# Kernel optimization log

Measured on AMD Instinct MI355X. Metric: run time of the kernel, lower is better.

The kernel has to match this reference:

```python
import jax, jax.numpy as jnp
import numpy as np

D = 1024        # hidden_size
H = 16          # num_heads
HD = D // H     # head_dim = 64
K = 4           # conv kernel size
I = int(D * 2.7)  # ffn intermediate = 2764
B, T = 2, 2048
EPS = 1e-6
GATE_BIAS = 4.0


def setup_inputs() -> dict:
    key = jax.random.key(0)
    ks = jax.random.split(key, 16)
    s = D ** -0.5
    return {
        "x": jax.random.normal(ks[0], (B, T, D), jnp.float32),
        "norm1_w": jnp.ones((D,), jnp.float32),
        "norm2_w": jnp.ones((D,), jnp.float32),
        "conv_w": jax.random.normal(ks[1], (D, K), jnp.float32) * 0.2,
        "conv_b": jnp.zeros((D,), jnp.float32),
        "wq": jax.random.normal(ks[2], (D, D), jnp.float32) * s,
        "wk": jax.random.normal(ks[3], (D, D), jnp.float32) * s,
        "wv": jax.random.normal(ks[4], (D, D), jnp.float32) * s,
        "wb": jax.random.normal(ks[5], (D, H), jnp.float32) * s,
        "wa": jax.random.normal(ks[6], (D, H), jnp.float32) * s,
        "wo": jax.random.normal(ks[7], (D, D), jnp.float32) * s,
        "wg": jax.random.normal(ks[8], (D, I), jnp.float32) * s,
        "wu": jax.random.normal(ks[9], (D, I), jnp.float32) * s,
        "wd": jax.random.normal(ks[10], (I, D), jnp.float32) * (I ** -0.5),
    }


def _rmsnorm(x, w):
    return x * jax.lax.rsqrt(jnp.mean(x * x, axis=-1, keepdims=True) + EPS) * w


def _causal_depthwise_conv(x, conv_w, conv_b):
    # x: [B,T,D]; depthwise causal conv, kernel K, then SiLU
    xt = jnp.transpose(x, (0, 2, 1))  # [B,D,T]
    y = jax.lax.conv_general_dilated(
        xt, conv_w[:, None, :],  # [D,1,K]
        window_strides=(1,), padding=[(K - 1, 0)],
        feature_group_count=D,
        dimension_numbers=("NCH", "OIH", "NCH"))
    y = jnp.transpose(y, (0, 2, 1)) + conv_b  # [B,T,D]
    return jax.nn.silu(y)


def _l2norm(x):
    return x * jax.lax.rsqrt(jnp.sum(x * x, axis=-1, keepdims=True) + EPS)


def _gated_delta_rule(xc, wq, wk, wv, wb, wa):
    b, t = xc.shape[0], xc.shape[1]
    q = _l2norm((xc @ wq).reshape(b, t, H, HD))
    k = _l2norm((xc @ wk).reshape(b, t, H, HD))
    v = (xc @ wv).reshape(b, t, H, HD)
    beta = jax.nn.sigmoid(xc @ wb)              # [B,T,H]
    alpha = jax.nn.sigmoid(xc @ wa + GATE_BIAS)  # [B,T,H] decay gate

    # time-major for scan
    qt = jnp.moveaxis(q, 1, 0)
    kt = jnp.moveaxis(k, 1, 0)
    vt = jnp.moveaxis(v, 1, 0)
    bt = jnp.moveaxis(beta, 1, 0)
    at = jnp.moveaxis(alpha, 1, 0)

    S0 = jnp.zeros((b, H, HD, HD), xc.dtype)  # [B,H,dk,dv]

    def step(S, inp):
        q_, k_, v_, b_, a_ = inp
        S = a_[..., None, None] * S
        pred = jnp.einsum("bhkv,bhk->bhv", S, k_)
        S = S + k_[..., :, None] * (b_[..., None] * (v_ - pred))[..., None, :]
        o = jnp.einsum("bhkv,bhk->bhv", S, q_)
        return S, o

    _, o = jax.lax.scan(step, S0, (qt, kt, vt, bt, at))  # [T,B,H,HD]
    return jnp.moveaxis(o, 1, 0).reshape(b, t, D)


def reference(x, norm1_w, norm2_w, conv_w, conv_b, wq, wk, wv, wb, wa, wo,
              wg, wu, wd):
    residual = x
    xn = _rmsnorm(x, norm1_w)
    xc = _causal_depthwise_conv(xn, conv_w, conv_b)
    mixer_out = _gated_delta_rule(xc, wq, wk, wv, wb, wa) @ wo
    h = residual + mixer_out
    hn = _rmsnorm(h, norm2_w)
    ffn = (jax.nn.silu(hn @ wg) * (hn @ wu)) @ wd
    return h + ffn
```

## Files before the change

### kernel.cpp

```cpp
#include <hip/hip_runtime.h>
#include <math.h>

#define D_ 1024
#define H_ 16
#define HD_ 64
#define KW_ 4
#define I_ 2764
#define IP_ 2816
#define NQKV_ 3200
#define NGU_ 5632
#define B_ 2
#define T_ 2048
#define BT_ (B_*T_)
#define ND_ (BT_*D_)
#define NH_ (BT_*H_)
#define NCH_ 32
#define NG_ (32*NCH_)
#define EPS_ 1e-6f
#define GATE_BIAS_ 4.0f

typedef __attribute__((ext_vector_type(8))) short bf16x8;
typedef __attribute__((ext_vector_type(4))) float f32x4;

#define MFMA_(a,b,c) __builtin_amdgcn_mfma_f32_16x16x32_bf16(a, b, c, 0, 0, 0)
#define GLDS_(src, dst) __builtin_amdgcn_global_load_lds( \
    (const __attribute__((address_space(1))) void*)(src), \
    (__attribute__((address_space(3))) void*)(dst), 16, 0, 0)

__device__ float f_sc1[BT_];
__device__ float f_be[NH_];
__device__ float f_al[NH_];
__device__ float f_h[ND_];
__device__ float g_rs[NG_ * 256];
__device__ float g_BmT[(size_t)NG_*4096];
__device__ unsigned short g_Gqk[(size_t)NG_*4096];
__device__ unsigned short g_Y[(size_t)NG_*4096];
__device__ unsigned short g_ZT[(size_t)NG_*4096];
__device__ unsigned short g_A[(size_t)NG_*4096];
__device__ unsigned short g_S[(size_t)NG_*4096];
__device__ unsigned short b_q[ND_];
__device__ unsigned short b_k[ND_];
__device__ unsigned short b_v[ND_];
__device__ unsigned short b_xc[ND_];
__device__ unsigned short b_o[ND_];
__device__ unsigned short b_hn[ND_];
__device__ unsigned short b_f[(size_t)BT_*IP_];
__device__ unsigned short b_wqkvT[(size_t)NQKV_*D_];
__device__ unsigned short b_woT[D_*D_];
__device__ unsigned short b_wguT[(size_t)NGU_*D_];
__device__ unsigned short b_wdT[(size_t)D_*IP_];

__device__ __forceinline__ unsigned short f2b(float x) {
  union { float f; unsigned u; } a; a.f = x;
  unsigned r = a.u + 0x7fff + ((a.u >> 16) & 1);
  return (unsigned short)(r >> 16);
}
__device__ __forceinline__ float b2f(unsigned short s) {
  union { unsigned u; float f; } a; a.u = ((unsigned)s) << 16; return a.f;
}

__device__ __forceinline__ const unsigned short* bsel(int id) {
  switch (id) {
    case 0: return b_xc;  case 1: return b_o;    case 2: return b_hn;
    case 3: return b_f;   case 4: return b_wqkvT; case 5: return b_woT;
    case 6: return b_wguT; default: return b_wdT;
  }
}
__device__ __forceinline__ unsigned short* bselw(int id) {
  return (unsigned short*)bsel(id);
}

__global__ __launch_bounds__(256) void rmssc_k(const float* __restrict__ x) {
  int row = blockIdx.x;
  int tid = threadIdx.x;
  float4 v = ((const float4*)(x + (size_t)row * D_))[tid];
  float ss = v.x*v.x + v.y*v.y + v.z*v.z + v.w*v.w;
  #pragma unroll
  for (int o = 32; o > 0; o >>= 1) ss += __shfl_down(ss, o);
  __shared__ float sred[4];
  if ((tid & 63) == 0) sred[tid >> 6] = ss;
  __syncthreads();
  if (tid == 0)
    f_sc1[row] = rsqrtf((sred[0]+sred[1]+sred[2]+sred[3]) / (float)D_ + EPS_);
}

__global__ __launch_bounds__(256) void rms2_k(const float* __restrict__ w) {
  int row = blockIdx.x;
  const float* xr = f_h + (size_t)row * D_;
  int tid = threadIdx.x;
  float4 v = ((const float4*)xr)[tid];
  float ss = v.x*v.x + v.y*v.y + v.z*v.z + v.w*v.w;
  #pragma unroll
  for (int o = 32; o > 0; o >>= 1) ss += __shfl_down(ss, o);
  __shared__ float sred[4];
  __shared__ float sscale;
  if ((tid & 63) == 0) sred[tid >> 6] = ss;
  __syncthreads();
  if (tid == 0)
    sscale = rsqrtf((sred[0]+sred[1]+sred[2]+sred[3]) / (float)D_ + EPS_);
  __syncthreads();
  float s = sscale;
  float4 wv = ((const float4*)w)[tid];
  unsigned short* orow = b_hn + (size_t)row * D_ + tid * 4;
  orow[0] = f2b(v.x*s*wv.x); orow[1] = f2b(v.y*s*wv.y);
  orow[2] = f2b(v.z*s*wv.z); orow[3] = f2b(v.w*s*wv.w);
}

__global__ __launch_bounds__(256) void conv2_k(const float* __restrict__ x,
                                               const float* __restrict__ cw,
                                               const float* __restrict__ cb,
                                               const float* __restrict__ n1w) {
  int idx = blockIdx.x * 256 + threadIdx.x;
  int d = idx & (D_ - 1);
  int bt = idx >> 10;
  int t = bt & (T_ - 1);
  float wd = n1w[d];
  float acc = cb[d];
  #pragma unroll
  for (int j = 0; j < KW_; j++) {
    int tt = t - (KW_ - 1) + j;
    if (tt >= 0) {
      int off = j - (KW_ - 1);
      acc += x[(size_t)idx + (size_t)off * D_] * f_sc1[bt + off] * wd * cw[d * KW_ + j];
    }
  }
  float s = acc / (1.f + expf(-acc));
  b_xc[idx] = f2b(s);
}

__global__ __launch_bounds__(256) void castTqkv_k(const float* __restrict__ wq,
                                                  const float* __restrict__ wk,
                                                  const float* __restrict__ wv,
                                                  const float* __restrict__ wb,
                                                  const float* __restrict__ wa) {
  __shared__ float s[64][65];
  int n0 = blockIdx.x * 64, k0 = blockIdx.y * 64;
  int tx = threadIdx.x & 63, ty = threadIdx.x >> 6;
  int nn = n0 + tx;
  const float* src = nullptr; int col = 0, ld = 1024;
  if (nn < 1024)      { src = wq; col = nn; }
  else if (nn < 2048) { src = wk; col = nn - 1024; }
  else if (nn < 3072) { src = wv; col = nn - 2048; }
  else if (nn < 3088) { src = wb; col = nn - 3072; ld = 16; }
  else if (nn < 3104) { src = wa; col = nn - 3088; ld = 16; }
  #pragma unroll
  for (int j = ty; j < 64; j += 4)
    s[j][tx] = src ? src[(size_t)(k0 + j) * ld + col] : 0.f;
  __syncthreads();
  #pragma unroll
  for (int j = ty; j < 64; j += 4)
    b_wqkvT[(size_t)(n0 + j) * D_ + k0 + tx] = f2b(s[tx][j]);
}

__global__ __launch_bounds__(256) void castTgu_k(const float* __restrict__ wg,
                                                 const float* __restrict__ wu) {
  __shared__ float s[64][65];
  int n0 = blockIdx.x * 64, k0 = blockIdx.y * 64;
  int tx = threadIdx.x & 63, ty = threadIdx.x >> 6;
  int nn = n0 + tx;
  int inner = nn & 31;
  int col = (nn >> 5) * 16 + (inner & 15);
  const float* src = (inner < 16) ? wg : wu;
  bool ok = (col < I_);
  #pragma unroll
  for (int j = ty; j < 64; j += 4)
    s[j][tx] = ok ? src[(size_t)(k0 + j) * I_ + col] : 0.f;
  __syncthreads();
  #pragma unroll
  for (int j = ty; j < 64; j += 4)
    b_wguT[(size_t)(n0 + j) * D_ + k0 + tx] = f2b(s[tx][j]);
}

__global__ __launch_bounds__(256) void castT_k(const float* __restrict__ W,
                                               int K, int N, int outid, int Kp) {
  __shared__ float s[64][65];
  unsigned short* out = bselw(outid);
  int k0 = blockIdx.y * 64, n0 = blockIdx.x * 64;
  int tx = threadIdx.x & 63, ty = threadIdx.x >> 6;
  #pragma unroll
  for (int j = ty; j < 64; j += 4) {
    int kk = k0 + j, nn = n0 + tx;
    s[j][tx] = (kk < K && nn < N) ? W[(size_t)kk * N + nn] : 0.f;
  }
  __syncthreads();
  #pragma unroll
  for (int j = ty; j < 64; j += 4)
    out[(size_t)(n0 + j) * Kp + k0 + tx] = f2b(s[tx][j]);
}

__global__ __launch_bounds__(256) void gemm_bf16(int aid, int bid, int Kp, int mode,
                                                 const float* __restrict__ ext,
                                                 float* __restrict__ eout) {
  __shared__ __align__(16) unsigned short Al[3][128 * 32];
  __shared__ __align__(16) unsigned short Bl[3][128 * 32];
  const unsigned short* A = bsel(aid);
  const unsigned short* Bt = bsel(bid);
  int tid = threadIdx.x;
  int nbx = gridDim.x;
  int nwg = nbx * gridDim.y;
  int lid = blockIdx.y * nbx + blockIdx.x;
  int cpx = nwg >> 3;
  int swzb = (lid & 7) * cpx + (lid >> 3);
  int m0 = (swzb / nbx) * 128, n0 = (swzb % nbx) * 128;
  int wave = tid >> 6, lane = tid & 63;
  int wm = (wave >> 1) * 64, wn = (wave & 1) * 64;
  int lrow = tid >> 2;
  int lcol = ((tid & 3) ^ ((lrow >> 1) & 3)) * 8;
  f32x4 acc[4][4] = {};
  const int l15 = lane & 15, lg = lane >> 4;
  const int sw = (lg ^ ((l15 >> 1) & 3)) * 8;
  const int nt = Kp >> 5;
  const unsigned short* Arow = A + (size_t)m0 * Kp;
  const unsigned short* Brow = Bt + (size_t)n0 * Kp;
  {
    GLDS_(Arow + (size_t)lrow * Kp + lcol,        Al[0] + wave * 512);
    GLDS_(Arow + (size_t)(64 + lrow) * Kp + lcol, Al[0] + 2048 + wave * 512);
    GLDS_(Brow + (size_t)lrow * Kp + lcol,        Bl[0] + wave * 512);
    GLDS_(Brow + (size_t)(64 + lrow) * Kp + lcol, Bl[0] + 2048 + wave * 512);
    GLDS_(Arow + (size_t)lrow * Kp + 32 + lcol,        Al[1] + wave * 512);
    GLDS_(Arow + (size_t)(64 + lrow) * Kp + 32 + lcol, Al[1] + 2048 + wave * 512);
    GLDS_(Brow + (size_t)lrow * Kp + 32 + lcol,        Bl[1] + wave * 512);
    GLDS_(Brow + (size_t)(64 + lrow) * Kp + 32 + lcol, Bl[1] + 2048 + wave * 512);
  }
  int c0i = 0, c1i = 1, c2i = 2;
  for (int t = 0; t < nt; t++) {
    if (t + 2 < nt) {
      int k0 = (t + 2) << 5;
      GLDS_(Arow + (size_t)lrow * Kp + k0 + lcol,        Al[c2i] + wave * 512);
      GLDS_(Arow + (size_t)(64 + lrow) * Kp + k0 + lcol, Al[c2i] + 2048 + wave * 512);
      GLDS_(Brow + (size_t)lrow * Kp + k0 + lcol,        Bl[c2i] + wave * 512);
      GLDS_(Brow + (size_t)(64 + lrow) * Kp + k0 + lcol, Bl[c2i] + 2048 + wave * 512);
      asm volatile("s_waitcnt vmcnt(8)" ::: "memory");
    } else if (t + 1 < nt) {
      asm volatile("s_waitcnt vmcnt(4)" ::: "memory");
    } else {
      asm volatile("s_waitcnt vmcnt(0)" ::: "memory");
    }
    __builtin_amdgcn_sched_barrier(0);
    __builtin_amdgcn_s_barrier();
    __builtin_amdgcn_sched_barrier(0);
    bf16x8 af[4], bf[4];
    #pragma unroll
    for (int i = 0; i < 4; i++)
      af[i] = *(const bf16x8*)&Al[c0i][(wm + i * 16 + l15) * 32 + sw];
    #pragma unroll
    for (int j = 0; j < 4; j++)
      bf[j] = *(const bf16x8*)&Bl[c0i][(wn + j * 16 + l15) * 32 + sw];
    #pragma unroll
    for (int i = 0; i < 4; i++)
      #pragma unroll
      for (int j = 0; j < 4; j++)
        acc[i][j] = MFMA_(af[i], bf[j], acc[i][j]);
    __builtin_amdgcn_sched_barrier(0);
    __builtin_amdgcn_s_barrier();
    __builtin_amdgcn_sched_barrier(0);
    int tmp = c0i; c0i = c1i; c1i = c2i; c2i = tmp;
  }
  int C0 = n0 + wn;
  if (mode == 0) {
    if (C0 < 2048) {
      unsigned short* dst = (C0 < 1024) ? b_q : b_k;
      int cbase = C0 & 1023;
      #pragma unroll
      for (int i = 0; i < 4; i++) {
        int r0i = m0 + wm + i * 16 + lg * 4;
        #pragma unroll
        for (int r = 0; r < 4; r++) {
          float ss = acc[i][0][r]*acc[i][0][r] + acc[i][1][r]*acc[i][1][r]
                   + acc[i][2][r]*acc[i][2][r] + acc[i][3][r]*acc[i][3][r];
          ss += __shfl_xor(ss, 1); ss += __shfl_xor(ss, 2);
          ss += __shfl_xor(ss, 4); ss += __shfl_xor(ss, 8);
          float sc = rsqrtf(ss + EPS_);
          #pragma unroll
          for (int j = 0; j < 4; j++)
            dst[(size_t)(r0i + r) * D_ + cbase + j * 16 + l15] = f2b(acc[i][j][r] * sc);
        }
      }
    } else if (C0 < 3072) {
      int cbase = C0 & 1023;
      #pragma unroll
      for (int i = 0; i < 4; i++) {
        int r0i = m0 + wm + i * 16 + lg * 4;
        #pragma unroll
        for (int j = 0; j < 4; j++)
          #pragma unroll
          for (int r = 0; r < 4; r++)
            b_v[(size_t)(r0i + r) * D_ + cbase + j * 16 + l15] = f2b(acc[i][j][r]);
      }
    } else if (C0 == 3072) {
      #pragma unroll
      for (int i = 0; i < 4; i++) {
        int r0i = m0 + wm + i * 16 + lg * 4;
        #pragma unroll
        for (int r = 0; r < 4; r++) {
          float vb = acc[i][0][r];
          f_be[(size_t)(r0i + r) * H_ + l15] = 1.f / (1.f + expf(-vb));
          float va = acc[i][1][r] + GATE_BIAS_;
          f_al[(size_t)(r0i + r) * H_ + l15] = 1.f / (1.f + expf(-va));
        }
      }
    }
  } else if (mode == 1) {
    #pragma unroll
    for (int i = 0; i < 4; i++) {
      int r0i = m0 + wm + i * 16 + lg * 4;
      #pragma unroll
      for (int jp = 0; jp < 2; jp++) {
        int j = jp * 2;
        int Lbase = ((C0 + j * 16) >> 5) * 16;
        #pragma unroll
        for (int r = 0; r < 4; r++) {
          float g = acc[i][j][r], u = acc[i][j + 1][r];
          float sg = g / (1.f + expf(-g));
          b_f[(size_t)(r0i + r) * IP_ + Lbase + l15] = f2b(sg * u);
        }
      }
    }
  } else if (mode == 2) {
    #pragma unroll
    for (int i = 0; i < 4; i++) {
      int r0i = m0 + wm + i * 16 + lg * 4;
      #pragma unroll
      for (int j = 0; j < 4; j++)
        #pragma unroll
        for (int r = 0; r < 4; r++) {
          size_t off = (size_t)(r0i + r) * D_ + C0 + j * 16 + l15;
          f_h[off] = ext[off] + acc[i][j][r];
        }
    }
  } else {
    #pragma unroll
    for (int i = 0; i < 4; i++) {
      int r0i = m0 + wm + i * 16 + lg * 4;
      #pragma unroll
      for (int j = 0; j < 4; j++)
        #pragma unroll
        for (int r = 0; r < 4; r++) {
          size_t off = (size_t)(r0i + r) * D_ + C0 + j * 16 + l15;
          eout[off] = f_h[off] + acc[i][j][r];
        }
    }
  }
}


__global__ __launch_bounds__(256) void prep_k() {
  __shared__ __align__(16) char sm[40448];
  unsigned short* sKT = (unsigned short*)sm;
  unsigned short* sVT = (unsigned short*)(sm + 10240);
  unsigned short* sAb = (unsigned short*)(sm + 20480);
  unsigned short* sYT = (unsigned short*)(sm + 20480);
  unsigned short* sXb = (unsigned short*)(sm + 29696);
  float* sL  = (float*)(sm + 38912);
  float* sB  = (float*)(sm + 39168);
  float* sS2 = (float*)(sm + 39424);
  float* sDec= (float*)(sm + 39680);
  float* sGC = (float*)(sm + 39936);

  int gid = blockIdx.x;
  int ch = gid & 31, bh = gid >> 5;
  int b = bh >> 4, h = bh & 15;
  int c0 = ch * 64, hb = h * HD_;
  int rowb = b * T_ + c0;
  int tid = threadIdx.x;
  int w = tid >> 6, lane = tid & 63, l15 = lane & 15, lg = lane >> 4;
  size_t g4 = (size_t)gid * 4096;

  if (tid < 64) {
    size_t rb = ((size_t)(rowb + tid)) * H_ + h;
    float la = log2f(f_al[rb]);
    #pragma unroll
    for (int m = 1; m < 64; m <<= 1) {
      float o = __shfl_up(la, m);
      if (tid >= m) la += o;
    }
    float L63 = __shfl(la, 63);
    float bt = f_be[rb];
    float g = exp2f(la);
    sL[tid] = la; sB[tid] = bt; sS2[tid] = bt * g;
    sDec[tid] = exp2f(L63 - la);
    if (tid == 63) sGC[0] = g;
    g_rs[(size_t)gid*256 + tid*4 + 0] = bt;
    g_rs[(size_t)gid*256 + tid*4 + 1] = bt * g;
    g_rs[(size_t)gid*256 + tid*4 + 2] = g;
  }
  __syncthreads();

  {
    int tp = tid >> 3, q8 = tid & 7;
    int t0 = 2 * tp, t1 = 2 * tp + 1;
    const bf16x8 k0 = *(const bf16x8*)(b_k + (size_t)(rowb + t0) * D_ + hb + q8 * 8);
    const bf16x8 k1 = *(const bf16x8*)(b_k + (size_t)(rowb + t1) * D_ + hb + q8 * 8);
    const bf16x8 v0 = *(const bf16x8*)(b_v + (size_t)(rowb + t0) * D_ + hb + q8 * 8);
    const bf16x8 v1 = *(const bf16x8*)(b_v + (size_t)(rowb + t1) * D_ + hb + q8 * 8);
    float s0 = sB[t0], s1v = sB[t1];
    unsigned* KT32 = (unsigned*)sKT;
    unsigned* VT32 = (unsigned*)sVT;
    #pragma unroll
    for (int i = 0; i < 8; i++) {
      int k = q8 * 8 + i;
      KT32[k*40 + tp] = (unsigned)(unsigned short)k0[i] |
                        ((unsigned)(unsigned short)k1[i] << 16);
      unsigned lo = f2b(b2f((unsigned short)v0[i]) * s0);
      unsigned hi = f2b(b2f((unsigned short)v1[i]) * s1v);
      VT32[k*40 + tp] = lo | (hi << 16);
    }
  }
  {
    bf16x8 bK[2], aK[4][2], aQ[4][2];
    #pragma unroll
    for (int k2 = 0; k2 < 2; k2++) {
      bK[k2] = *(const bf16x8*)&b_k[(size_t)(rowb + w*16 + l15)*D_ + hb + k2*32 + lg*8];
      #pragma unroll
      for (int ti = 0; ti < 4; ti++) {
        aK[ti][k2] = *(const bf16x8*)&b_k[(size_t)(rowb + ti*16 + l15)*D_ + hb + k2*32 + lg*8];
        aQ[ti][k2] = *(const bf16x8*)&b_q[(size_t)(rowb + ti*16 + l15)*D_ + hb + k2*32 + lg*8];
      }
    }
    f32x4 ck[4] = {}, cq[4] = {};
    #pragma unroll
    for (int k2 = 0; k2 < 2; k2++)
      #pragma unroll
      for (int ti = 0; ti < 4; ti++) {
        ck[ti] = MFMA_(aK[ti][k2], bK[k2], ck[ti]);
        cq[ti] = MFMA_(aQ[ti][k2], bK[k2], cq[ti]);
      }
    int j = w*16 + l15;
    float Lj = sL[j];
    #pragma unroll
    for (int ti = 0; ti < 4; ti++)
      #pragma unroll
      for (int r = 0; r < 4; r++) {
        int t = ti*16 + lg*4 + r;
        float ratio = exp2f(sL[t] - Lj);
        sAb[t*72 + j] = f2b((j < t) ? sB[t] * ratio * ck[ti][r] : 0.f);
        g_Gqk[g4 + t*64 + j] = f2b((j <= t) ? ratio * cq[ti][r] : 0.f);
      }
  }
  __syncthreads();
  {
    int c = (w << 4) + (lane >> 2);
    int p = lane & 3;
    int rb16 = p << 4;
    float xr[16];
    #pragma unroll
    for (int j = 0; j < 16; j++) xr[j] = 0.f;
    #pragma unroll
    for (int q = 0; q < 16; q++) {
      int r0 = 4 * q;
      const unsigned short* abr = sAb + r0 * 72 + rb16;
      bf16x8 A0a = *(const bf16x8*)(abr);
      bf16x8 A0b = *(const bf16x8*)(abr + 8);
      bf16x8 A1a = *(const bf16x8*)(abr + 72);
      bf16x8 A1b = *(const bf16x8*)(abr + 80);
      bf16x8 A2a = *(const bf16x8*)(abr + 144);
      bf16x8 A2b = *(const bf16x8*)(abr + 152);
      bf16x8 A3a = *(const bf16x8*)(abr + 216);
      bf16x8 A3b = *(const bf16x8*)(abr + 224);
      float s0 = 0.f, s1 = 0.f, s2 = 0.f, s3 = 0.f;
      #pragma unroll
      for (int j = 0; j < 8; j++) {
        float xv = xr[j], xw = xr[8 + j];
        s0 = fmaf(b2f((unsigned short)A0a[j]), xv, s0);
        s1 = fmaf(b2f((unsigned short)A1a[j]), xv, s1);
        s2 = fmaf(b2f((unsigned short)A2a[j]), xv, s2);
        s3 = fmaf(b2f((unsigned short)A3a[j]), xv, s3);
        s0 = fmaf(b2f((unsigned short)A0b[j]), xw, s0);
        s1 = fmaf(b2f((unsigned short)A1b[j]), xw, s1);
        s2 = fmaf(b2f((unsigned short)A2b[j]), xw, s2);
        s3 = fmaf(b2f((unsigned short)A3b[j]), xw, s3);
      }
      s0 += __shfl_xor(s0, 1); s0 += __shfl_xor(s0, 2);
      s1 += __shfl_xor(s1, 1); s1 += __shfl_xor(s1, 2);
      s2 += __shfl_xor(s2, 1); s2 += __shfl_xor(s2, 2);
      s3 += __shfl_xor(s3, 1); s3 += __shfl_xor(s3, 2);
      float a10 = b2f(sAb[(r0+1)*72 + r0]);
      float a20 = b2f(sAb[(r0+2)*72 + r0]);
      float a21 = b2f(sAb[(r0+2)*72 + r0+1]);
      float a30 = b2f(sAb[(r0+3)*72 + r0]);
      float a31 = b2f(sAb[(r0+3)*72 + r0+1]);
      float a32 = b2f(sAb[(r0+3)*72 + r0+2]);
      float x0 = ((r0+0) == c ? 1.f : 0.f) - s0;
      float x1 = ((r0+1) == c ? 1.f : 0.f) - s1 - a10*x0;
      float x2 = ((r0+2) == c ? 1.f : 0.f) - s2 - a20*x0 - a21*x1;
      float x3 = ((r0+3) == c ? 1.f : 0.f) - s3 - a30*x0 - a31*x1 - a32*x2;
      if (p == (q >> 2)) {
        int ji = 4 * (q & 3);
        xr[ji+0] = x0; xr[ji+1] = x1; xr[ji+2] = x2; xr[ji+3] = x3;
      }
    }
    #pragma unroll
    for (int j = 0; j < 16; j++)
      sXb[(rb16 + j)*72 + c] = f2b(xr[j]);
  }
  __syncthreads();
  int m0 = w * 16;
  f32x4 cyT[4], cz[4];
  {
    bf16x8 aKT[2];
    aKT[0] = *(const bf16x8*)&sKT[(m0 + l15)*80 + lg*8];
    aKT[1] = *(const bf16x8*)&sKT[(m0 + l15)*80 + 32 + lg*8];
    #pragma unroll
    for (int n = 0; n < 4; n++) {
      cyT[n] = f32x4{0.f, 0.f, 0.f, 0.f};
      #pragma unroll
      for (int k2 = 0; k2 < 2; k2++) {
        bf16x8 bb;
        #pragma unroll
        for (int i = 0; i < 8; i++) {
          int tp = k2*32 + lg*8 + i;
          bb[i] = (short)f2b(b2f(sXb[(n*16 + l15)*72 + tp]) * sS2[tp]);
        }
        cyT[n] = MFMA_(aKT[k2], bb, cyT[n]);
      }
    }
    bf16x8 aT2[2];
    #pragma unroll
    for (int k2 = 0; k2 < 2; k2++)
      #pragma unroll
      for (int i = 0; i < 8; i++) {
        int tp = k2*32 + lg*8 + i;
        aT2[k2][i] = (short)f2b(b2f(sXb[(m0 + l15)*72 + tp]) * sS2[tp]);
      }
    #pragma unroll
    for (int n = 0; n < 4; n++) {
      f32x4 c = {};
      #pragma unroll
      for (int k2 = 0; k2 < 2; k2++) {
        bf16x8 bKT = *(const bf16x8*)&sKT[(n*16 + l15)*80 + k2*32 + lg*8];
        c = MFMA_(aT2[k2], bKT, c);
      }
      #pragma unroll
      for (int r = 0; r < 4; r++)
        g_Y[g4 + (m0 + lg*4 + r)*64 + n*16 + l15] = f2b(c[r]);
    }
    bf16x8 aV[2];
    aV[0] = *(const bf16x8*)&sVT[(m0 + l15)*80 + lg*8];
    aV[1] = *(const bf16x8*)&sVT[(m0 + l15)*80 + 32 + lg*8];
    #pragma unroll
    for (int n = 0; n < 4; n++) {
      cz[n] = f32x4{0.f, 0.f, 0.f, 0.f};
      #pragma unroll
      for (int k2 = 0; k2 < 2; k2++) {
        bf16x8 bT = *(const bf16x8*)&sXb[(n*16 + l15)*72 + k2*32 + lg*8];
        cz[n] = MFMA_(aV[k2], bT, cz[n]);
      }
      #pragma unroll
      for (int r = 0; r < 4; r++)
        g_ZT[g4 + (m0 + lg*4 + r)*64 + n*16 + l15] = f2b(cz[n][r]);
    }
  }
  __syncthreads();
  #pragma unroll
  for (int n = 0; n < 4; n++)
    #pragma unroll
    for (int r = 0; r < 4; r++) {
      sYT[(m0 + lg*4 + r)*72 + n*16 + l15] = f2b(cyT[n][r]);
      sVT[(m0 + lg*4 + r)*80 + n*16 + l15] = f2b(cz[n][r]);
    }
  {
    int xx = tid >> 2, q = tid & 3;
    bf16x8 v0 = *(const bf16x8*)&sKT[xx*80 + q*16];
    bf16x8 v1 = *(const bf16x8*)&sKT[xx*80 + q*16 + 8];
    bf16x8 d0, d1;
    #pragma unroll
    for (int i = 0; i < 8; i++) {
      d0[i] = (short)f2b(b2f((unsigned short)v0[i]) * sDec[q*16 + i]);
      d1[i] = (short)f2b(b2f((unsigned short)v1[i]) * sDec[q*16 + 8 + i]);
    }
    *(bf16x8*)&sKT[xx*80 + q*16] = d0;
    *(bf16x8*)&sKT[xx*80 + q*16 + 8] = d1;
  }
  __syncthreads();
  {
    float gC = sGC[0];
    bf16x8 aKd[2];
    aKd[0] = *(const bf16x8*)&sKT[(m0 + l15)*80 + lg*8];
    aKd[1] = *(const bf16x8*)&sKT[(m0 + l15)*80 + 32 + lg*8];
    #pragma unroll
    for (int n = 0; n < 4; n++) {
      f32x4 c = {};
      #pragma unroll
      for (int k2 = 0; k2 < 2; k2++) {
        bf16x8 bY = *(const bf16x8*)&sYT[(n*16 + l15)*72 + k2*32 + lg*8];
        c = MFMA_(aKd[k2], bY, c);
      }
      #pragma unroll
      for (int r = 0; r < 4; r++) {
        int row = m0 + lg*4 + r, col = n*16 + l15;
        g_A[g4 + row*64 + col] = f2b(((row == col) ? gC : 0.f) - c[r]);
      }
    }
    #pragma unroll
    for (int n = 0; n < 4; n++) {
      f32x4 c = {};
      #pragma unroll
      for (int k2 = 0; k2 < 2; k2++) {
        bf16x8 bZ = *(const bf16x8*)&sVT[(n*16 + l15)*80 + k2*32 + lg*8];
        c = MFMA_(aKd[k2], bZ, c);
      }
      *(f32x4*)&g_BmT[g4 + (size_t)(n*16 + l15)*64 + m0 + lg*4] = c;
    }
  }
}

__global__ __launch_bounds__(256) void seq_k() {
  __shared__ __align__(16) unsigned short sST[4][16*80];
  int bh = blockIdx.x;
  int tid = threadIdx.x, w = tid >> 6, lane = tid & 63;
  int l15 = lane & 15, lg = lane >> 4;
  unsigned short* st = sST[w];
  for (int i = lane; i < 16*80; i += 64) st[i] = 0;
  f32x4 cerr[4] = {};
  bf16x8 aA[4][2];
  f32x4 cini[4];
  size_t g40 = (size_t)(bh * 32) * 4096;
  #pragma unroll
  for (int m = 0; m < 4; m++) {
    aA[m][0] = *(const bf16x8*)&g_A[g40 + (m*16 + l15)*64 + lg*8];
    aA[m][1] = *(const bf16x8*)&g_A[g40 + (m*16 + l15)*64 + 32 + lg*8];
    cini[m] = *(const f32x4*)&g_BmT[g40 + (w*16 + l15)*64 + m*16 + lg*4];
  }
  for (int ch = 0; ch < NCH_; ch++) {
    size_t gid = (size_t)bh * 32 + ch;
    float gC = g_rs[gid*256 + 254];
    bf16x8 bS0 = *(const bf16x8*)&st[l15*80 + lg*8];
    bf16x8 bS1 = *(const bf16x8*)&st[l15*80 + 32 + lg*8];
    *(bf16x8*)&g_S[gid*4096 + (w*16 + l15)*64 + lg*8] = bS0;
    *(bf16x8*)&g_S[gid*4096 + (w*16 + l15)*64 + 32 + lg*8] = bS1;
    bf16x8 aAn[4][2];
    f32x4 cin2[4];
    if (ch + 1 < NCH_) {
      size_t g4n = (gid + 1) * 4096;
      #pragma unroll
      for (int m = 0; m < 4; m++) {
        aAn[m][0] = *(const bf16x8*)&g_A[g4n + (m*16 + l15)*64 + lg*8];
        aAn[m][1] = *(const bf16x8*)&g_A[g4n + (m*16 + l15)*64 + 32 + lg*8];
        cin2[m] = *(const f32x4*)&g_BmT[g4n + (w*16 + l15)*64 + m*16 + lg*4];
      }
    }
    f32x4 c[4];
    #pragma unroll
    for (int m = 0; m < 4; m++) {
      #pragma unroll
      for (int r = 0; r < 4; r++)
        c[m][r] = cini[m][r] + gC * cerr[m][r];
      c[m] = MFMA_(aA[m][0], bS0, c[m]);
      c[m] = MFMA_(aA[m][1], bS1, c[m]);
    }
    #pragma unroll
    for (int m = 0; m < 4; m++)
      #pragma unroll
      for (int r = 0; r < 4; r++) {
        float x = c[m][r];
        unsigned short q = f2b(x);
        cerr[m][r] = x - b2f(q);
        st[l15*80 + m*16 + lg*4 + r] = q;
      }
    if (ch + 1 < NCH_) {
      #pragma unroll
      for (int m = 0; m < 4; m++) {
        aA[m][0] = aAn[m][0]; aA[m][1] = aAn[m][1];
        cini[m] = cin2[m];
      }
    }
  }
}

__global__ __launch_bounds__(256) void apply_k() {
  __shared__ __align__(16) unsigned short sUT[4][16*80];
  int gid = blockIdx.x;
  int ch = gid & 31, bh = gid >> 5;
  int b = bh >> 4, h = bh & 15;
  int c0 = ch * 64, hb = h * HD_;
  int rowb = b * T_ + c0;
  int tid = threadIdx.x, w = tid >> 6, lane = tid & 63;
  int l15 = lane & 15, lg = lane >> 4;
  unsigned short* ut = sUT[w];
  size_t g4 = (size_t)gid * 4096;
  bf16x8 aS[2];
  aS[0] = *(const bf16x8*)&g_S[g4 + (w*16 + l15)*64 + lg*8];
  aS[1] = *(const bf16x8*)&g_S[g4 + (w*16 + l15)*64 + 32 + lg*8];
  f32x4 cu[4];
  #pragma unroll
  for (int n = 0; n < 4; n++) {
    cu[n] = f32x4{0.f, 0.f, 0.f, 0.f};
    #pragma unroll
    for (int k2 = 0; k2 < 2; k2++) {
      bf16x8 bY = *(const bf16x8*)&g_Y[g4 + (n*16 + l15)*64 + k2*32 + lg*8];
      cu[n] = MFMA_(aS[k2], bY, cu[n]);
    }
  }
  #pragma unroll
  for (int n = 0; n < 4; n++)
    #pragma unroll
    for (int r = 0; r < 4; r++) {
      float zt = b2f(g_ZT[g4 + (w*16 + lg*4 + r)*64 + n*16 + l15]);
      ut[(lg*4 + r)*80 + n*16 + l15] = f2b(zt - cu[n][r]);
    }
  bf16x8 aU[2];
  aU[0] = *(const bf16x8*)&ut[l15*80 + lg*8];
  aU[1] = *(const bf16x8*)&ut[l15*80 + 32 + lg*8];
  f32x4 co[4];
  #pragma unroll
  for (int n = 0; n < 4; n++) {
    co[n] = f32x4{0.f, 0.f, 0.f, 0.f};
    #pragma unroll
    for (int k2 = 0; k2 < 2; k2++) {
      bf16x8 bQ = *(const bf16x8*)&b_q[(size_t)(rowb + n*16 + l15)*D_ + hb + k2*32 + lg*8];
      co[n] = MFMA_(aS[k2], bQ, co[n]);
    }
    float gm = g_rs[(size_t)gid*256 + (n*16 + l15)*4 + 2];
    #pragma unroll
    for (int r = 0; r < 4; r++) co[n][r] *= gm;
    #pragma unroll
    for (int k2 = 0; k2 < 2; k2++) {
      bf16x8 bG = *(const bf16x8*)&g_Gqk[g4 + (n*16 + l15)*64 + k2*32 + lg*8];
      co[n] = MFMA_(aU[k2], bG, co[n]);
    }
    ushort4 pk;
    pk.x = f2b(co[n][0]); pk.y = f2b(co[n][1]);
    pk.z = f2b(co[n][2]); pk.w = f2b(co[n][3]);
    *(ushort4*)&b_o[(size_t)(rowb + n*16 + l15)*D_ + hb + w*16 + lg*4] = pk;
  }
}

extern "C" void kernel_launch(void* const* d_in, const int* in_sizes, int n_in,
                              void* d_out, int out_size, void* d_ws, size_t ws_size,
                              hipStream_t stream) {
  const float* x   = (const float*)d_in[0];
  const float* n1w = (const float*)d_in[1];
  const float* n2w = (const float*)d_in[2];
  const float* cw  = (const float*)d_in[3];
  const float* cb  = (const float*)d_in[4];
  const float* wq  = (const float*)d_in[5];
  const float* wk  = (const float*)d_in[6];
  const float* wv  = (const float*)d_in[7];
  const float* wb  = (const float*)d_in[8];
  const float* wa  = (const float*)d_in[9];
  const float* wo  = (const float*)d_in[10];
  const float* wg  = (const float*)d_in[11];
  const float* wu  = (const float*)d_in[12];
  const float* wd  = (const float*)d_in[13];
  float* out = (float*)d_out;

  castTqkv_k<<<dim3(50, 16), 256, 0, stream>>>(wq, wk, wv, wb, wa);
  castT_k<<<dim3(16, 16), 256, 0, stream>>>(wo, D_, D_, 5, D_);
  castTgu_k<<<dim3(88, 16), 256, 0, stream>>>(wg, wu);
  castT_k<<<dim3(16, 44), 256, 0, stream>>>(wd, I_, D_, 7, IP_);

  rmssc_k<<<BT_, 256, 0, stream>>>(x);
  conv2_k<<<ND_ / 256, 256, 0, stream>>>(x, cw, cb, n1w);

  gemm_bf16<<<dim3(25, 32), 256, 0, stream>>>(0, 4, D_, 0, nullptr, nullptr);

  prep_k<<<NG_, 256, 0, stream>>>();
  seq_k<<<32, 256, 0, stream>>>();
  apply_k<<<NG_, 256, 0, stream>>>();

  gemm_bf16<<<dim3(8, 32), 256, 0, stream>>>(1, 5, D_, 2, x, nullptr);
  rms2_k<<<BT_, 256, 0, stream>>>(n2w);
  gemm_bf16<<<dim3(44, 32), 256, 0, stream>>>(2, 6, D_, 1, nullptr, nullptr);
  gemm_bf16<<<dim3(8, 32), 256, 0, stream>>>(3, 7, IP_, 3, nullptr, out);
}
```

Before: 465.2 us.

## Load GEMM B operand directly from global into registers, bypassing LDS

The GEMM kernel no longer stages the B (weight) tile through shared memory. Each wave loads its own B fragments straight from global memory into registers, double-buffered across two k-steps, while A still goes through a triple-buffered LDS pipeline. The aim is to halve LDS traffic and footprint and raise occupancy. In exchange, B reads become duplicated across waves sharing the same columns and uncoalesced (16-byte per lane, strided rows), and the vmcnt accounting now mixes register and LDS loads, with an implicit assumption that nt is even.

After: 512.6 us. 10.2% more time.

```diff
diff --git a/kernel.cpp b/kernel.cpp
--- a/kernel.cpp
+++ b/kernel.cpp
@@ -192,7 +192,6 @@
                                                  const float* __restrict__ ext,
                                                  float* __restrict__ eout) {
   __shared__ __align__(16) unsigned short Al[3][128 * 32];
-  __shared__ __align__(16) unsigned short Bl[3][128 * 32];
   const unsigned short* A = bsel(aid);
   const unsigned short* Bt = bsel(bid);
   int tid = threadIdx.x;
@@ -211,50 +210,79 @@
   const int sw = (lg ^ ((l15 >> 1) & 3)) * 8;
   const int nt = Kp >> 5;
   const unsigned short* Arow = A + (size_t)m0 * Kp;
-  const unsigned short* Brow = Bt + (size_t)n0 * Kp;
-  {
-    GLDS_(Arow + (size_t)lrow * Kp + lcol,        Al[0] + wave * 512);
-    GLDS_(Arow + (size_t)(64 + lrow) * Kp + lcol, Al[0] + 2048 + wave * 512);
-    GLDS_(Brow + (size_t)lrow * Kp + lcol,        Bl[0] + wave * 512);
-    GLDS_(Brow + (size_t)(64 + lrow) * Kp + lcol, Bl[0] + 2048 + wave * 512);
-    GLDS_(Arow + (size_t)lrow * Kp + 32 + lcol,        Al[1] + wave * 512);
-    GLDS_(Arow + (size_t)(64 + lrow) * Kp + 32 + lcol, Al[1] + 2048 + wave * 512);
-    GLDS_(Brow + (size_t)lrow * Kp + 32 + lcol,        Bl[1] + wave * 512);
-    GLDS_(Brow + (size_t)(64 + lrow) * Kp + 32 + lcol, Bl[1] + 2048 + wave * 512);
-  }
-  int c0i = 0, c1i = 1, c2i = 2;
-  for (int t = 0; t < nt; t++) {
-    if (t + 2 < nt) {
-      int k0 = (t + 2) << 5;
-      GLDS_(Arow + (size_t)lrow * Kp + k0 + lcol,        Al[c2i] + wave * 512);
-      GLDS_(Arow + (size_t)(64 + lrow) * Kp + k0 + lcol, Al[c2i] + 2048 + wave * 512);
-      GLDS_(Brow + (size_t)lrow * Kp + k0 + lcol,        Bl[c2i] + wave * 512);
-      GLDS_(Brow + (size_t)(64 + lrow) * Kp + k0 + lcol, Bl[c2i] + 2048 + wave * 512);
-      asm volatile("s_waitcnt vmcnt(8)" ::: "memory");
-    } else if (t + 1 < nt) {
-      asm volatile("s_waitcnt vmcnt(4)" ::: "memory");
-    } else {
-      asm volatile("s_waitcnt vmcnt(0)" ::: "memory");
-    }
-    __builtin_amdgcn_sched_barrier(0);
-    __builtin_amdgcn_s_barrier();
-    __builtin_amdgcn_sched_barrier(0);
-    bf16x8 af[4], bf[4];
-    #pragma unroll
-    for (int i = 0; i < 4; i++)
-      af[i] = *(const bf16x8*)&Al[c0i][(wm + i * 16 + l15) * 32 + sw];
-    #pragma unroll
-    for (int j = 0; j < 4; j++)
-      bf[j] = *(const bf16x8*)&Bl[c0i][(wn + j * 16 + l15) * 32 + sw];
-    #pragma unroll
-    for (int i = 0; i < 4; i++)
+  const unsigned short* Brow[4];
+  #pragma unroll
+  for (int j = 0; j < 4; j++)
+    Brow[j] = Bt + (size_t)(n0 + wn + j * 16 + l15) * Kp + lg * 8;
+  bf16x8 bA[4], bB[4];
+  GLDS_(Arow + (size_t)lrow * Kp + lcol,        Al[0] + wave * 512);
+  GLDS_(Arow + (size_t)(64 + lrow) * Kp + lcol, Al[0] + 2048 + wave * 512);
+  GLDS_(Arow + (size_t)lrow * Kp + 32 + lcol,        Al[1] + wave * 512);
+  GLDS_(Arow + (size_t)(64 + lrow) * Kp + 32 + lcol, Al[1] + 2048 + wave * 512);
+  #pragma unroll
+  for (int j = 0; j < 4; j++) bA[j] = *(const bf16x8*)(Brow[j]);
+  for (int t = 0; t < nt; t += 2) {
+    {
       #pragma unroll
       for (int j = 0; j < 4; j++)
-        acc[i][j] = MFMA_(af[i], bf[j], acc[i][j]);
-    __builtin_amdgcn_sched_barrier(0);
-    __builtin_amdgcn_s_barrier();
-    __builtin_amdgcn_sched_barrier(0);
-    int tmp = c0i; c0i = c1i; c1i = c2i; c2i = tmp;
+        bB[j] = *(const bf16x8*)(Brow[j] + (t + 1) * 32);
+      if (t + 2 < nt) {
+        int k0 = (t + 2) << 5;
+        unsigned short* dst = Al[(t + 2) % 3];
+        GLDS_(Arow + (size_t)lrow * Kp + k0 + lcol,        dst + wave * 512);
+        GLDS_(Arow + (size_t)(64 + lrow) * Kp + k0 + lcol, dst + 2048 + wave * 512);
+        asm volatile("s_waitcnt vmcnt(6)" ::: "memory");
+      } else {
+        asm volatile("s_waitcnt vmcnt(4)" ::: "memory");
+      }
+      __builtin_amdgcn_sched_barrier(0);
+      __builtin_amdgcn_s_barrier();
+      __builtin_amdgcn_sched_barrier(0);
+      const unsigned short* Ab = Al[t % 3];
+      bf16x8 af[4];
+      #pragma unroll
+      for (int i = 0; i < 4; i++)
+        af[i] = *(const bf16x8*)&Ab[(wm + i * 16 + l15) * 32 + sw];
+      #pragma unroll
+      for (int i = 0; i < 4; i++)
+        #pragma unroll
+        for (int j = 0; j < 4; j++)
+          acc[i][j] = MFMA_(af[i], bA[j], acc[i][j]);
+      __builtin_amdgcn_sched_barrier(0);
+      __builtin_amdgcn_s_barrier();
+      __builtin_amdgcn_sched_barrier(0);
+    }
+    {
+      int tt = t + 1;
+      if (tt + 1 < nt) {
+        #pragma unroll
+        for (int j = 0; j < 4; j++)
+          bA[j] = *(const bf16x8*)(Brow[j] + (tt + 1) * 32);
+        int k0 = (tt + 2) << 5;
+        unsigned short* dst = Al[(tt + 2) % 3];
+        GLDS_(Arow + (size_t)lrow * Kp + k0 + lcol,        dst + wave * 512);
+        GLDS_(Arow + (size_t)(64 + lrow) * Kp + k0 + lcol, dst + 2048 + wave * 512);
+        asm volatile("s_waitcnt vmcnt(6)" ::: "memory");
+      } else {
+        asm volatile("s_waitcnt vmcnt(0)" ::: "memory");
+      }
+      __builtin_amdgcn_sched_barrier(0);
+      __builtin_amdgcn_s_barrier();
+      __builtin_amdgcn_sched_barrier(0);
+      const unsigned short* Ab = Al[tt % 3];
+      bf16x8 af[4];
+      #pragma unroll
+      for (int i = 0; i < 4; i++)
+        af[i] = *(const bf16x8*)&Ab[(wm + i * 16 + l15) * 32 + sw];
+      #pragma unroll
+      for (int i = 0; i < 4; i++)
+        #pragma unroll
+        for (int j = 0; j < 4; j++)
+          acc[i][j] = MFMA_(af[i], bB[j], acc[i][j]);
+      __builtin_amdgcn_sched_barrier(0);
+      __builtin_amdgcn_s_barrier();
+      __builtin_amdgcn_sched_barrier(0);
+    }
   }
   int C0 = n0 + wn;
   if (mode == 0) {
```

## Add 256x256-tile 512-thread GEMM for QKV and gate/up projections

Applied to the files above, without the earlier changes.

Adds a new bf16 MFMA GEMM kernel with 256x256 output tiles, 8 waves, K-step 64, double-buffered LDS filled by direct global-to-LDS loads, and raised wave priority around the MFMA block. The QKV projection and the gate/up projection move to this kernel, with the QKV weight padding raised so N divides into 256-wide tiles. Their fused epilogues move out of the old GEMM. Larger tiles raise operand reuse per LDS load and halve the block count, at the cost of more LDS and registers per block, lower occupancy, and fewer blocks to spread across the compute units.

After: 433.9 us (median of 2 runs). 6.7% less time.

```diff
diff --git a/kernel.cpp b/kernel.cpp
--- a/kernel.cpp
+++ b/kernel.cpp
@@ -7,7 +7,7 @@
 #define KW_ 4
 #define I_ 2764
 #define IP_ 2816
-#define NQKV_ 3200
+#define NQKV_ 3328
 #define NGU_ 5632
 #define B_ 2
 #define T_ 2048
@@ -186,6 +186,143 @@
   #pragma unroll
   for (int j = ty; j < 64; j += 4)
     out[(size_t)(n0 + j) * Kp + k0 + tx] = f2b(s[tx][j]);
+}
+
+__global__ __launch_bounds__(512) void gemm256(int aid, int bid, int Kp, int mode) {
+  __shared__ __align__(16) unsigned short Al[2][256 * 64];
+  __shared__ __align__(16) unsigned short Bl[2][256 * 64];
+  const unsigned short* A = bsel(aid);
+  const unsigned short* Bt = bsel(bid);
+  int tid = threadIdx.x;
+  int nbx = gridDim.x;
+  int nwg = nbx * gridDim.y;
+  int lid = blockIdx.y * nbx + blockIdx.x;
+  int cpx = nwg >> 3;
+  int swzb = (lid & 7) * cpx + (lid >> 3);
+  int m0 = (swzb / nbx) * 256, n0 = (swzb % nbx) * 256;
+  int w = tid >> 6, lane = tid & 63;
+  int wm = (w >> 2) * 128, wn = (w & 3) * 64;
+  const int l15 = lane & 15, lg = lane >> 4;
+  int srow = tid >> 3;
+  int scol = ((tid & 7) ^ (srow & 7)) * 8;
+  int ldsw = w * 512;
+  const unsigned short* Arow = A + (size_t)m0 * Kp;
+  const unsigned short* Brow = Bt + (size_t)n0 * Kp;
+  int swz0 = ((0 + lg) ^ (l15 & 7)) * 8;
+  int swz1 = ((4 + lg) ^ (l15 & 7)) * 8;
+  f32x4 acc[8][4] = {};
+  const int nt = Kp >> 6;
+  #pragma unroll
+  for (int i = 0; i < 4; i++) {
+    GLDS_(Arow + (size_t)(i * 64 + srow) * Kp + scol, Al[0] + i * 4096 + ldsw);
+    GLDS_(Brow + (size_t)(i * 64 + srow) * Kp + scol, Bl[0] + i * 4096 + ldsw);
+  }
+  asm volatile("s_waitcnt vmcnt(0)" ::: "memory");
+  __builtin_amdgcn_s_barrier();
+  int cur = 0;
+  for (int t = 0; t < nt; t++) {
+    if (t + 1 < nt) {
+      int k0 = (t + 1) << 6;
+      #pragma unroll
+      for (int i = 0; i < 4; i++) {
+        GLDS_(Arow + (size_t)(i * 64 + srow) * Kp + k0 + scol, Al[cur ^ 1] + i * 4096 + ldsw);
+        GLDS_(Brow + (size_t)(i * 64 + srow) * Kp + k0 + scol, Bl[cur ^ 1] + i * 4096 + ldsw);
+      }
+    }
+    __builtin_amdgcn_s_setprio(1);
+    {
+      bf16x8 af[8], bf[4];
+      #pragma unroll
+      for (int i = 0; i < 8; i++)
+        af[i] = *(const bf16x8*)&Al[cur][(wm + i * 16 + l15) * 64 + swz0];
+      #pragma unroll
+      for (int j = 0; j < 4; j++)
+        bf[j] = *(const bf16x8*)&Bl[cur][(wn + j * 16 + l15) * 64 + swz0];
+      #pragma unroll
+      for (int i = 0; i < 8; i++)
+        #pragma unroll
+        for (int j = 0; j < 4; j++)
+          acc[i][j] = MFMA_(af[i], bf[j], acc[i][j]);
+      #pragma unroll
+      for (int i = 0; i < 8; i++)
+        af[i] = *(const bf16x8*)&Al[cur][(wm + i * 16 + l15) * 64 + swz1];
+      #pragma unroll
+      for (int j = 0; j < 4; j++)
+        bf[j] = *(const bf16x8*)&Bl[cur][(wn + j * 16 + l15) * 64 + swz1];
+      #pragma unroll
+      for (int i = 0; i < 8; i++)
+        #pragma unroll
+        for (int j = 0; j < 4; j++)
+          acc[i][j] = MFMA_(af[i], bf[j], acc[i][j]);
+    }
+    __builtin_amdgcn_s_setprio(0);
+    __builtin_amdgcn_sched_barrier(0);
+    asm volatile("s_waitcnt vmcnt(0)" ::: "memory");
+    __builtin_amdgcn_s_barrier();
+    __builtin_amdgcn_sched_barrier(0);
+    cur ^= 1;
+  }
+  int C0 = n0 + wn;
+  if (mode == 0) {
+    if (C0 < 2048) {
+      unsigned short* dst = (C0 < 1024) ? b_q : b_k;
+      int cbase = C0 & 1023;
+      #pragma unroll
+      for (int i = 0; i < 8; i++) {
+        int r0i = m0 + wm + i * 16 + lg * 4;
+        #pragma unroll
+        for (int r = 0; r < 4; r++) {
+          float ss = acc[i][0][r]*acc[i][0][r] + acc[i][1][r]*acc[i][1][r]
+                   + acc[i][2][r]*acc[i][2][r] + acc[i][3][r]*acc[i][3][r];
+          ss += __shfl_xor(ss, 1); ss += __shfl_xor(ss, 2);
+          ss += __shfl_xor(ss, 4); ss += __shfl_xor(ss, 8);
+          float sc = rsqrtf(ss + EPS_);
+          #pragma unroll
+          for (int j = 0; j < 4; j++)
+            dst[(size_t)(r0i + r) * D_ + cbase + j * 16 + l15] = f2b(acc[i][j][r] * sc);
+        }
+      }
+    } else if (C0 < 3072) {
+      int cbase = C0 & 1023;
+      #pragma unroll
+      for (int i = 0; i < 8; i++) {
+        int r0i = m0 + wm + i * 16 + lg * 4;
+        #pragma unroll
+        for (int j = 0; j < 4; j++)
+          #pragma unroll
+          for (int r = 0; r < 4; r++)
+            b_v[(size_t)(r0i + r) * D_ + cbase + j * 16 + l15] = f2b(acc[i][j][r]);
+      }
+    } else if (C0 == 3072) {
+      #pragma unroll
+      for (int i = 0; i < 8; i++) {
+        int r0i = m0 + wm + i * 16 + lg * 4;
+        #pragma unroll
+        for (int r = 0; r < 4; r++) {
+          float vb = acc[i][0][r];
+          f_be[(size_t)(r0i + r) * H_ + l15] = 1.f / (1.f + expf(-vb));
+          float va = acc[i][1][r] + GATE_BIAS_;
+          f_al[(size_t)(r0i + r) * H_ + l15] = 1.f / (1.f + expf(-va));
+        }
+      }
+    }
+  } else {
+    #pragma unroll
+    for (int i = 0; i < 8; i++) {
+      int r0i = m0 + wm + i * 16 + lg * 4;
+      #pragma unroll
+      for (int jp = 0; jp < 2; jp++) {
+        int j = jp * 2;
+        int Lbase = ((C0 + j * 16) >> 5) * 16;
+        #pragma unroll
+        for (int r = 0; r < 4; r++) {
+          float g = acc[i][j][r], u = acc[i][j + 1][r];
+          float sg = g / (1.f + expf(-g));
+          b_f[(size_t)(r0i + r) * IP_ + Lbase + l15] = f2b(sg * u);
+        }
+      }
+    }
+  }
 }
 
 __global__ __launch_bounds__(256) void gemm_bf16(int aid, int bid, int Kp, int mode,
@@ -257,66 +394,7 @@
     int tmp = c0i; c0i = c1i; c1i = c2i; c2i = tmp;
   }
   int C0 = n0 + wn;
-  if (mode == 0) {
-    if (C0 < 2048) {
-      unsigned short* dst = (C0 < 1024) ? b_q : b_k;
-      int cbase = C0 & 1023;
-      #pragma unroll
-      for (int i = 0; i < 4; i++) {
-        int r0i = m0 + wm + i * 16 + lg * 4;
-        #pragma unroll
-        for (int r = 0; r < 4; r++) {
-          float ss = acc[i][0][r]*acc[i][0][r] + acc[i][1][r]*acc[i][1][r]
-                   + acc[i][2][r]*acc[i][2][r] + acc[i][3][r]*acc[i][3][r];
-          ss += __shfl_xor(ss, 1); ss += __shfl_xor(ss, 2);
-          ss += __shfl_xor(ss, 4); ss += __shfl_xor(ss, 8);
-          float sc = rsqrtf(ss + EPS_);
-          #pragma unroll
-          for (int j = 0; j < 4; j++)
-            dst[(size_t)(r0i + r) * D_ + cbase + j * 16 + l15] = f2b(acc[i][j][r] * sc);
-        }
-      }
-    } else if (C0 < 3072) {
-      int cbase = C0 & 1023;
-      #pragma unroll
-      for (int i = 0; i < 4; i++) {
-        int r0i = m0 + wm + i * 16 + lg * 4;
-        #pragma unroll
-        for (int j = 0; j < 4; j++)
-          #pragma unroll
-          for (int r = 0; r < 4; r++)
-            b_v[(size_t)(r0i + r) * D_ + cbase + j * 16 + l15] = f2b(acc[i][j][r]);
-      }
-    } else if (C0 == 3072) {
-      #pragma unroll
-      for (int i = 0; i < 4; i++) {
-        int r0i = m0 + wm + i * 16 + lg * 4;
-        #pragma unroll
-        for (int r = 0; r < 4; r++) {
-          float vb = acc[i][0][r];
-          f_be[(size_t)(r0i + r) * H_ + l15] = 1.f / (1.f + expf(-vb));
-          float va = acc[i][1][r] + GATE_BIAS_;
-          f_al[(size_t)(r0i + r) * H_ + l15] = 1.f / (1.f + expf(-va));
-        }
-      }
-    }
-  } else if (mode == 1) {
-    #pragma unroll
-    for (int i = 0; i < 4; i++) {
-      int r0i = m0 + wm + i * 16 + lg * 4;
-      #pragma unroll
-      for (int jp = 0; jp < 2; jp++) {
-        int j = jp * 2;
-        int Lbase = ((C0 + j * 16) >> 5) * 16;
-        #pragma unroll
-        for (int r = 0; r < 4; r++) {
-          float g = acc[i][j][r], u = acc[i][j + 1][r];
-          float sg = g / (1.f + expf(-g));
-          b_f[(size_t)(r0i + r) * IP_ + Lbase + l15] = f2b(sg * u);
-        }
-      }
-    }
-  } else if (mode == 2) {
+  if (mode == 2) {
     #pragma unroll
     for (int i = 0; i < 4; i++) {
       int r0i = m0 + wm + i * 16 + lg * 4;
@@ -744,7 +822,7 @@
   const float* wd  = (const float*)d_in[13];
   float* out = (float*)d_out;
 
-  castTqkv_k<<<dim3(50, 16), 256, 0, stream>>>(wq, wk, wv, wb, wa);
+  castTqkv_k<<<dim3(52, 16), 256, 0, stream>>>(wq, wk, wv, wb, wa);
   castT_k<<<dim3(16, 16), 256, 0, stream>>>(wo, D_, D_, 5, D_);
   castTgu_k<<<dim3(88, 16), 256, 0, stream>>>(wg, wu);
   castT_k<<<dim3(16, 44), 256, 0, stream>>>(wd, I_, D_, 7, IP_);
@@ -752,7 +830,7 @@
   rmssc_k<<<BT_, 256, 0, stream>>>(x);
   conv2_k<<<ND_ / 256, 256, 0, stream>>>(x, cw, cb, n1w);
 
-  gemm_bf16<<<dim3(25, 32), 256, 0, stream>>>(0, 4, D_, 0, nullptr, nullptr);
+  gemm256<<<dim3(13, 16), 512, 0, stream>>>(0, 4, D_, 0);
 
   prep_k<<<NG_, 256, 0, stream>>>();
   seq_k<<<32, 256, 0, stream>>>();
@@ -760,6 +838,6 @@
 
   gemm_bf16<<<dim3(8, 32), 256, 0, stream>>>(1, 5, D_, 2, x, nullptr);
   rms2_k<<<BT_, 256, 0, stream>>>(n2w);
-  gemm_bf16<<<dim3(44, 32), 256, 0, stream>>>(2, 6, D_, 1, nullptr, nullptr);
+  gemm256<<<dim3(22, 16), 512, 0, stream>>>(2, 6, D_, 1);
   gemm_bf16<<<dim3(8, 32), 256, 0, stream>>>(3, 7, IP_, 3, nullptr, out);
 }
```
